# Kernel tuning notes

Hardware: AMD Instinct MI355X
Metric: run time of the kernel (lower is better)

Reference implementation:

```python
import jax, jax.numpy as jnp
import numpy as np

EMBED = 256; DEPTH = 64; DEPTH_START = 1.0
POS_RANGE = (-61.2, -61.2, -10.0, 61.2, 61.2, 10.0)
PC_RANGE = (-51.2, -51.2, -5.0, 51.2, 51.2, 3.0)
MEM_LEN = 512; TOPK = 256; NUM_Q = 900; NUM_CLS = 10; CODE = 10; L = 6
B, N, H, W = 4, 6, 16, 44
PAD_H, PAD_W = 256, 704
TWO_PI = 2.0 * np.pi


def _posemb(coords, nf=128):
    # sine/cosine embedding per coordinate channel -> [..., C, nf]
    dim_t = 10000.0 ** (2.0 * (jnp.arange(nf, dtype=jnp.float32) // 2) / nf)
    p = (coords * TWO_PI)[..., None] / dim_t
    p = jnp.stack([jnp.sin(p[..., 0::2]), jnp.cos(p[..., 1::2])], -1)
    return p.reshape(p.shape[:-2] + (nf,))


def _mlp2(x, W1, b1, W2, b2):
    return jnp.maximum(x @ W1 + b1, 0.0) @ W2 + b2


def _conv1x1(x, Wt, b):
    return jnp.einsum('bchw,co->bohw', x, Wt) + b[None, :, None, None]


def _ln(x, g, b):
    m = jnp.mean(x, -1, keepdims=True)
    v = jnp.mean(jnp.square(x - m), -1, keepdims=True)
    return (x - m) / jnp.sqrt(v + 1e-5) * g + b


def _sine_pe(not_mask):
    # SinePositionalEncoding2D, normalize=True; not_mask: [BN,H,W] float
    nf = EMBED // 2; eps = 1e-6
    y = jnp.cumsum(not_mask, 1); x = jnp.cumsum(not_mask, 2)
    y = y / (y[:, -1:, :] + eps) * TWO_PI
    x = x / (x[:, :, -1:] + eps) * TWO_PI
    dim_t = 10000.0 ** (2.0 * (jnp.arange(nf, dtype=jnp.float32) // 2) / nf)
    px = x[..., None] / dim_t; py = y[..., None] / dim_t
    px = jnp.stack([jnp.sin(px[..., 0::2]), jnp.cos(px[..., 1::2])], -1).reshape(x.shape + (nf,))
    py = jnp.stack([jnp.sin(py[..., 0::2]), jnp.cos(py[..., 1::2])], -1).reshape(y.shape + (nf,))
    return jnp.concatenate([py, px], -1).transpose(0, 3, 1, 2)  # [BN,EMBED,H,W]


def _forward(feat, lidar2img, prev_exists, memory_embedding, memory_reference_point,
             memory_timestamp, outs_dec, ref_pts, ip_w, ip_b, pe_w1, pe_b1, pe_w2, pe_b2,
             ap_w1, ap_b1, ap_w2, ap_b2, qe_w1, qe_b1, qe_w2, qe_b2, te_w1, te_b1, te_w2,
             te_b2, cls_w1, cls_b1, cls_g1, cls_be1, cls_w2, cls_b2, cls_g2, cls_be2,
             cls_w3, cls_b3, reg_w1, reg_b1, reg_w2, reg_b2, reg_w3, reg_b3, masks):
    b, n, c, h, w = feat.shape
    # --- pre_update_memory: memory_refresh + timestamp advance ---
    prev = prev_exists.reshape(b, 1, 1)
    mem_e = memory_embedding * prev
    mem_r = memory_reference_point * prev
    mem_t = memory_timestamp * prev + prev
    # --- input projection (1x1 conv) ---
    x = _conv1x1(feat.reshape(b * n, c, h, w), ip_w, ip_b).reshape(b, n, EMBED, h, w)
    # --- 3D position embedding (PETR frustum) ---
    coords_h = jnp.arange(h, dtype=jnp.float32) * (float(PAD_H) / h)
    coords_w = jnp.arange(w, dtype=jnp.float32) * (float(PAD_W) / w)
    d = jnp.arange(DEPTH, dtype=jnp.float32)
    bin_size = (POS_RANGE[3] - DEPTH_START) / (DEPTH * (1.0 + DEPTH))
    coords_d = DEPTH_START + bin_size * d * (d + 1.0)  # LID discretization
    cw, ch_, cd = jnp.meshgrid(coords_w, coords_h, coords_d, indexing='ij')  # [W,H,D]
    xy = jnp.stack([cw, ch_], -1) * jnp.maximum(cd, 1e-5)[..., None]
    coords4 = jnp.concatenate([xy, cd[..., None], jnp.ones_like(cd[..., None])], -1)  # [W,H,D,4]
    img2lidars = jnp.linalg.inv(lidar2img)  # [B,N,4,4]
    c3 = jnp.einsum('bnij,whdj->bnwhdi', img2lidars, coords4)[..., :3]  # [B,N,W,H,D,3]
    lo = jnp.asarray(POS_RANGE[:3], jnp.float32); hi = jnp.asarray(POS_RANGE[3:], jnp.float32)
    c3 = (c3 - lo) / (hi - lo)
    cmask = ((c3 > 1.0) | (c3 < 0.0)).reshape(b, n, w, h, DEPTH * 3).sum(-1) > DEPTH * 0.5
    coords_mask = masks | cmask.transpose(0, 1, 3, 2)
    c3 = c3.transpose(0, 1, 4, 5, 3, 2).reshape(b * n, DEPTH * 3, h, w)
    c3 = jnp.clip(c3, 0.0, 1.0)
    c3 = jnp.log(jnp.clip(c3, 1e-5, None) / jnp.clip(1.0 - c3, 1e-5, None))  # inverse_sigmoid
    coords_pos = _conv1x1(jnp.maximum(_conv1x1(c3, pe_w1, pe_b1), 0.0), pe_w2, pe_b2)
    coords_pos = coords_pos.reshape(b, n, EMBED, h, w)
    # --- 2D sine PE + adapt_pos3d ---
    sine = _sine_pe((~masks).astype(jnp.float32).reshape(b * n, h, w))
    sine = _conv1x1(jnp.maximum(_conv1x1(sine, ap_w1, ap_b1), 0.0), ap_w2, ap_b2)
    pos_embed = coords_pos + sine.reshape(b, n, EMBED, h, w)
    # --- query / time embeddings ---
    qp = _posemb(ref_pts)  # [Q,3,128]
    qp = jnp.concatenate([qp[:, 1], qp[:, 0], qp[:, 2]], -1)  # (y,x,z) -> [Q,384]
    query_pos = _mlp2(qp, qe_w1, qe_b1, qe_w2, qe_b2)  # [Q,256]
    tp = _posemb(mem_t)[..., 0, :]  # [B,M,128]
    time_emb = _mlp2(tp, te_w1, te_b1, te_w2, te_b2)  # [B,M,256]
    # --- cls / reg branches, stacked over decoder layers ---
    hc = jnp.maximum(_ln(jnp.einsum('lbqd,lde->lbqe', outs_dec, cls_w1) + cls_b1[:, None, None], cls_g1[:, None, None], cls_be1[:, None, None]), 0.0)
    hc = jnp.maximum(_ln(jnp.einsum('lbqd,lde->lbqe', hc, cls_w2) + cls_b2[:, None, None], cls_g2[:, None, None], cls_be2[:, None, None]), 0.0)
    all_cls = jnp.einsum('lbqd,ldc->lbqc', hc, cls_w3) + cls_b3[:, None, None]
    hr = jnp.maximum(jnp.einsum('lbqd,lde->lbqe', outs_dec, reg_w1) + reg_b1[:, None, None], 0.0)
    hr = jnp.maximum(jnp.einsum('lbqd,lde->lbqe', hr, reg_w2) + reg_b2[:, None, None], 0.0)
    all_reg = jnp.einsum('lbqd,ldc->lbqc', hr, reg_w3) + reg_b3[:, None, None]
    # --- post_update_memory: sigmoid + topk + gather + rolling concat ---
    rec_score = jnp.max(jax.nn.sigmoid(all_cls[-1]), -1)  # topk(1) over classes == max
    _, idx = jax.lax.top_k(rec_score, TOPK)  # [B,K]
    rec_mem = jax.lax.stop_gradient(jnp.take_along_axis(outs_dec[-1], idx[..., None], axis=1))
    rec_ref = jax.lax.stop_gradient(jnp.take_along_axis(all_reg[-1][..., :3], idx[..., None], axis=1))
    pmin = jnp.asarray(PC_RANGE[:3], jnp.float32); pmax = jnp.asarray(PC_RANGE[3:], jnp.float32)
    rec_ref = jnp.clip((rec_ref - pmin) / jnp.clip(pmax - pmin, 1e-5, None), 0.0, 1.0)
    rec_ts = jnp.zeros((b, TOPK, 1), rec_mem.dtype)
    new_mem_e = jnp.concatenate([rec_mem, mem_e], 1)[:, :MEM_LEN]
    new_mem_r = jnp.concatenate([rec_ref, mem_r], 1)[:, :MEM_LEN]
    new_mem_t = jnp.concatenate([rec_ts, mem_t], 1)[:, :MEM_LEN]
    return (all_cls, all_reg, new_mem_e, new_mem_r, new_mem_t, pos_embed, x, query_pos, time_emb, coords_mask)


def setup_inputs() -> dict:
    key = jax.random.key(0)
    ks = jax.random.split(key, 24)
    def rn(k, shape, s=0.02):
        return jax.random.normal(k, shape, jnp.float32) * s
    inp = dict(
        feat=jax.random.normal(ks[0], (B, N, 256, H, W), jnp.float32),
        lidar2img=jnp.eye(4, dtype=jnp.float32) + 0.05 * jax.random.normal(ks[1], (B, N, 4, 4), jnp.float32),
        prev_exists=jnp.array([1.0, 0.0, 1.0, 1.0], jnp.float32),
        memory_embedding=jax.random.normal(ks[2], (B, MEM_LEN, EMBED), jnp.float32),
        memory_reference_point=jax.random.uniform(ks[3], (B, MEM_LEN, 3)),
        memory_timestamp=jax.random.uniform(ks[4], (B, MEM_LEN, 1)),
        outs_dec=jax.random.normal(ks[5], (L, B, NUM_Q, EMBED), jnp.float32),
        ref_pts=jax.random.uniform(ks[6], (NUM_Q, 3)),
        ip_w=rn(ks[7], (256, EMBED)), ip_b=jnp.zeros(EMBED),
        pe_w1=rn(ks[8], (3 * DEPTH, EMBED * 2)), pe_b1=jnp.zeros(EMBED * 2),
        pe_w2=rn(ks[9], (EMBED * 2, EMBED)), pe_b2=jnp.zeros(EMBED),
        ap_w1=rn(ks[10], (EMBED, EMBED)), ap_b1=jnp.zeros(EMBED),
        ap_w2=rn(ks[11], (EMBED, EMBED)), ap_b2=jnp.zeros(EMBED),
        qe_w1=rn(ks[12], (EMBED * 3 // 2, EMBED)), qe_b1=jnp.zeros(EMBED),
        qe_w2=rn(ks[13], (EMBED, EMBED)), qe_b2=jnp.zeros(EMBED),
        te_w1=rn(ks[14], (EMBED // 2, EMBED)), te_b1=jnp.zeros(EMBED),
        te_w2=rn(ks[15], (EMBED, EMBED)), te_b2=jnp.zeros(EMBED),
        cls_w1=rn(ks[16], (L, EMBED, EMBED)), cls_b1=jnp.zeros((L, EMBED)),
        cls_g1=jnp.ones((L, EMBED)), cls_be1=jnp.zeros((L, EMBED)),
        cls_w2=rn(ks[17], (L, EMBED, EMBED)), cls_b2=jnp.zeros((L, EMBED)),
        cls_g2=jnp.ones((L, EMBED)), cls_be2=jnp.zeros((L, EMBED)),
        cls_w3=rn(ks[18], (L, EMBED, NUM_CLS)), cls_b3=jnp.zeros((L, NUM_CLS)),
        reg_w1=rn(ks[19], (L, EMBED, EMBED)), reg_b1=jnp.zeros((L, EMBED)),
        reg_w2=rn(ks[20], (L, EMBED, EMBED)), reg_b2=jnp.zeros((L, EMBED)),
        reg_w3=rn(ks[21], (L, EMBED, CODE)), reg_b3=jnp.zeros((L, CODE)),
        masks=jnp.zeros((B, N, H, W), bool),
    )
    return inp


def reference(feat, lidar2img, prev_exists, memory_embedding, memory_reference_point,
              memory_timestamp, outs_dec, ref_pts, ip_w, ip_b, pe_w1, pe_b1, pe_w2, pe_b2,
              ap_w1, ap_b1, ap_w2, ap_b2, qe_w1, qe_b1, qe_w2, qe_b2, te_w1, te_b1, te_w2,
              te_b2, cls_w1, cls_b1, cls_g1, cls_be1, cls_w2, cls_b2, cls_g2, cls_be2,
              cls_w3, cls_b3, reg_w1, reg_b1, reg_w2, reg_b2, reg_w3, reg_b3, masks):
    return _forward(feat, lidar2img, prev_exists, memory_embedding, memory_reference_point,
                    memory_timestamp, outs_dec, ref_pts, ip_w, ip_b, pe_w1, pe_b1, pe_w2, pe_b2,
                    ap_w1, ap_b1, ap_w2, ap_b2, qe_w1, qe_b1, qe_w2, qe_b2, te_w1, te_b1, te_w2,
                    te_b2, cls_w1, cls_b1, cls_g1, cls_be1, cls_w2, cls_b2, cls_g2, cls_be2,
                    cls_w3, cls_b3, reg_w1, reg_b1, reg_w2, reg_b2, reg_w3, reg_b3, masks)
```

## Files before the change

kernel.cpp:

```cpp
#include <hip/hip_runtime.h>
#include <math.h>


typedef unsigned short u16;
typedef __attribute__((ext_vector_type(8))) short short8v;
typedef __attribute__((ext_vector_type(4))) float f32x4;

#define DI __device__ __forceinline__
DI u16 f2bf(float f) {
    unsigned x = __float_as_uint(f);
    return (u16)((x + 0x7fffu + ((x >> 16) & 1u)) >> 16);
}
DI float bf2f(u16 u) { return __uint_as_float(((unsigned)u) << 16); }

#define TWO_PI_F 6.283185307179586f

__global__ void k_inv(const float* __restrict__ l2i, float* __restrict__ out) {
    int t = threadIdx.x;
    if (t >= 24) return;
    float a[4][8];
    for (int i = 0; i < 4; i++)
        for (int j = 0; j < 4; j++) {
            a[i][j] = l2i[t * 16 + i * 4 + j];
            a[i][4 + j] = (i == j) ? 1.f : 0.f;
        }
    for (int c = 0; c < 4; c++) {
        int p = c; float mv = fabsf(a[c][c]);
        for (int r = c + 1; r < 4; r++) {
            float v = fabsf(a[r][c]);
            if (v > mv) { mv = v; p = r; }
        }
        if (p != c)
            for (int j = 0; j < 8; j++) { float tmp = a[c][j]; a[c][j] = a[p][j]; a[p][j] = tmp; }
        float ip = 1.f / a[c][c];
        for (int j = 0; j < 8; j++) a[c][j] *= ip;
        for (int r = 0; r < 4; r++) {
            if (r == c) continue;
            float f = a[r][c];
            for (int j = 0; j < 8; j++) a[r][j] -= f * a[c][j];
        }
    }
    for (int i = 0; i < 4; i++)
        for (int j = 0; j < 4; j++)
            out[t * 16 + i * 4 + j] = a[i][4 + j];
}

__global__ __launch_bounds__(256) void k_memtail(
    const float* __restrict__ me, const float* __restrict__ mr, const float* __restrict__ mt,
    const float* __restrict__ prev,
    float* __restrict__ oe, float* __restrict__ orr, float* __restrict__ ot) {
    int b = blockIdx.x >> 8, j = blockIdx.x & 255, o = threadIdx.x;
    float pv = prev[b];
    oe[(size_t)(b * 512 + 256 + j) * 256 + o] = me[(size_t)(b * 512 + j) * 256 + o] * pv;
    if (o < 3)
        orr[(size_t)(b * 512 + 256 + j) * 3 + o] = mr[(size_t)(b * 512 + j) * 3 + o] * pv;
    if (o == 0) {
        ot[b * 512 + 256 + j] = mt[b * 512 + j] * pv + pv;
        ot[b * 512 + j] = 0.f;
    }
}

__global__ __launch_bounds__(256) void k_frustum(
    const float* __restrict__ inv, u16* __restrict__ c3aT, float* __restrict__ cm) {
    int pix = blockIdx.x * 4 + (threadIdx.x >> 6);
    int d = threadIdx.x & 63;
    int bn = pix / 704, p = pix - bn * 704;
    int h = p / 44, w = p - h * 44;
    const float* M = inv + bn * 16;
    float cw = w * 16.0f, ch = h * 16.0f;
    const float bin = (61.2f - 1.0f) / (64.0f * 65.0f);
    float cd = 1.0f + (bin * d) * (d + 1.0f);
    float xx = cw * cd, yy = ch * cd;
    float px = M[0] * xx + M[1] * yy + M[2] * cd + M[3];
    float py = M[4] * xx + M[5] * yy + M[6] * cd + M[7];
    float pz = M[8] * xx + M[9] * yy + M[10] * cd + M[11];
    float c[3];
    c[0] = (px + 61.2f) * (1.f / 122.4f);
    c[1] = (py + 61.2f) * (1.f / 122.4f);
    c[2] = (pz + 10.0f) * (1.f / 20.0f);
    u16* o = c3aT + (size_t)pix * 192 + d * 3;
    int cnt = 0;
#pragma unroll
    for (int i = 0; i < 3; i++) {
        cnt += ((c[i] > 1.0f) || (c[i] < 0.0f)) ? 1 : 0;
        float cc = fminf(fmaxf(c[i], 0.f), 1.f);
        float num = fmaxf(cc, 1e-5f);
        float den = fmaxf(1.0f - cc, 1e-5f);
        o[i] = f2bf(logf(num / den));
    }
    for (int off = 32; off; off >>= 1) cnt += __shfl_down(cnt, off);
    if (d == 0) cm[pix] = (cnt > 32) ? 1.f : 0.f;
}

__global__ __launch_bounds__(256) void k_sinebase(float* __restrict__ out) {
    int idx = blockIdx.x * 256 + threadIdx.x;
    if (idx >= 256 * 704) return;
    int c = idx / 704, p = idx - c * 704;
    int h = p / 44, w = p - h * 44;
    float pos = (c < 128) ? (h + 1) * (TWO_PI_F / (16.0f + 1e-6f))
                          : (w + 1) * (TWO_PI_F / (44.0f + 1e-6f));
    int cc = c & 127, k = cc >> 1;
    float dt = powf(10000.f, k * (1.f / 64.f));
    float arg = pos / dt;
    out[idx] = (cc & 1) ? cosf(arg) : sinf(arg);
}

template <int MODE>
DI void mlp_body(int blk, const float* __restrict__ src, const float* __restrict__ prev,
                 const float* __restrict__ w1, const float* __restrict__ b1,
                 const float* __restrict__ w2, const float* __restrict__ b2,
                 float* __restrict__ out,
                 float (*finT)[16], float (*h1T)[20], float (*Ws)[256]) {
    constexpr int KF = MODE ? 384 : 128;
    constexpr int T1 = KF / 32;
    constexpr int MROWS = MODE ? 900 : 2048;
    const int tid = threadIdx.x;
    const int r0 = blk * 16;
    const int w4 = (tid >> 6) * 4;
    const int c4 = (tid & 63) * 4;

    for (int i = tid; i < 16 * KF; i += 256) {
        int r = i & 15, f = i >> 4;
        int row = r0 + r;
        int rs = (row < MROWS) ? row : (MROWS - 1);
        float arg;
        int fl;
        if (MODE == 0) {
            float pv = prev[rs >> 9];
            float mt = src[rs] * pv + pv;
            float dt = powf(10000.f, (f >> 1) * (1.f / 64.f));
            arg = mt * TWO_PI_F / dt;
            fl = f;
        } else {
            int seg = f >> 7, ff = f & 127;
            int cidx = (seg == 0) ? 1 : ((seg == 1) ? 0 : 2);
            float rv = src[rs * 3 + cidx];
            float dt = powf(10000.f, (ff >> 1) * (1.f / 64.f));
            arg = rv * TWO_PI_F / dt;
            fl = ff;
        }
        finT[f][r] = (fl & 1) ? cosf(arg) : sinf(arg);
    }

    auto stage = [&](const float* __restrict__ W, int t) {
        const float4* W4 = (const float4*)(W + (size_t)t * 32 * 256);
        float4* S4 = (float4*)Ws;
        float4 tmp[8];
#pragma unroll
        for (int j = 0; j < 8; j++) tmp[j] = W4[tid + j * 256];
#pragma unroll
        for (int j = 0; j < 8; j++) S4[tid + j * 256] = tmp[j];
    };

    float acc1[4][4] = {};
    for (int t = 0; t < T1; t++) {
        stage(w1, t);
        __syncthreads();
#pragma unroll 4
        for (int k = 0; k < 32; k++) {
            float4 fv = *(const float4*)&finT[t * 32 + k][w4];
            float4 wv = *(const float4*)&Ws[k][c4];
            float fa[4] = {fv.x, fv.y, fv.z, fv.w};
            float wa[4] = {wv.x, wv.y, wv.z, wv.w};
#pragma unroll
            for (int i = 0; i < 4; i++)
#pragma unroll
                for (int j = 0; j < 4; j++) acc1[i][j] = fmaf(fa[i], wa[j], acc1[i][j]);
        }
        __syncthreads();
    }
    {
        float4 bv = *(const float4*)&b1[c4];
        float ba[4] = {bv.x, bv.y, bv.z, bv.w};
#pragma unroll
        for (int i = 0; i < 4; i++)
#pragma unroll
            for (int j = 0; j < 4; j++)
                h1T[c4 + j][w4 + i] = fmaxf(acc1[i][j] + ba[j], 0.f);
    }

    float acc2[4][4] = {};
    for (int t = 0; t < 8; t++) {
        stage(w2, t);
        __syncthreads();
#pragma unroll 4
        for (int k = 0; k < 32; k++) {
            float4 fv = *(const float4*)&h1T[t * 32 + k][w4];
            float4 wv = *(const float4*)&Ws[k][c4];
            float fa[4] = {fv.x, fv.y, fv.z, fv.w};
            float wa[4] = {wv.x, wv.y, wv.z, wv.w};
#pragma unroll
            for (int i = 0; i < 4; i++)
#pragma unroll
                for (int j = 0; j < 4; j++) acc2[i][j] = fmaf(fa[i], wa[j], acc2[i][j]);
        }
        __syncthreads();
    }
    {
        float4 bv = *(const float4*)&b2[c4];
#pragma unroll
        for (int i = 0; i < 4; i++) {
            int row = r0 + w4 + i;
            if (row >= MROWS) continue;
            float4 o4;
            o4.x = acc2[i][0] + bv.x;
            o4.y = acc2[i][1] + bv.y;
            o4.z = acc2[i][2] + bv.z;
            o4.w = acc2[i][3] + bv.w;
            *(float4*)&out[(size_t)row * 256 + c4] = o4;
        }
    }
}

__global__ __launch_bounds__(256) void k_mlp2(
    const float* __restrict__ memt, const float* __restrict__ prev,
    const float* __restrict__ te_w1, const float* __restrict__ te_b1,
    const float* __restrict__ te_w2, const float* __restrict__ te_b2,
    float* __restrict__ o_te,
    const float* __restrict__ rp,
    const float* __restrict__ qe_w1, const float* __restrict__ qe_b1,
    const float* __restrict__ qe_w2, const float* __restrict__ qe_b2,
    float* __restrict__ o_qp) {
    __shared__ __align__(16) float finT[384][16];
    __shared__ __align__(16) float h1T[256][20];
    __shared__ __align__(16) float Ws[32][256];
    int blk = blockIdx.x;
    if (blk < 128)
        mlp_body<0>(blk, memt, prev, te_w1, te_b1, te_w2, te_b2, o_te, finT, h1T, Ws);
    else
        mlp_body<1>(blk - 128, rp, prev, qe_w1, qe_b1, qe_w2, qe_b2, o_qp, finT, h1T, Ws);
}

__global__ __launch_bounds__(256) void k_wtr4(
    const float* __restrict__ s0, const float* __restrict__ s1,
    const float* __restrict__ s2, const float* __restrict__ s3,
    u16* __restrict__ d0, u16* __restrict__ d1, u16* __restrict__ d2, u16* __restrict__ d3,
    int K, int N, int zper) {
    __shared__ float sh[32][33];
    int z = blockIdx.z, ti = z / zper, zz = z - ti * zper;
    const float* src = (ti == 0 ? s0 : ti == 1 ? s1 : ti == 2 ? s2 : s3) + (size_t)zz * K * N;
    u16* dst = (ti == 0 ? d0 : ti == 1 ? d1 : ti == 2 ? d2 : d3) + (size_t)zz * K * N;
    int n0 = blockIdx.x * 32, k0 = blockIdx.y * 32;
    int tx = threadIdx.x & 31, ty = threadIdx.x >> 5;
#pragma unroll
    for (int r = 0; r < 4; r++)
        sh[ty + 8 * r][tx] = src[(size_t)(k0 + ty + 8 * r) * N + n0 + tx];
    __syncthreads();
#pragma unroll
    for (int r = 0; r < 4; r++)
        dst[(size_t)(n0 + ty + 8 * r) * K + k0 + tx] = f2bf(sh[tx][ty + 8 * r]);
}

template <int AF32, int BTRANS, int BF32, int OUTF32, int ADD, int BIASM>
__global__ __launch_bounds__(256) void k_mfma(
    const void* __restrict__ Av, const void* __restrict__ B1v, const void* __restrict__ B2v,
    const float* __restrict__ bias1, const float* __restrict__ bias2,
    const float* __restrict__ add, void* __restrict__ outv,
    int M, int N, int K, int lda, int ldb, int ldo,
    long aZ, long bZ, long biasZ, long oZ, int zsplit, int zrelu, int aFull) {
    __shared__ __align__(16) u16 As[64][40];
    __shared__ __align__(16) u16 Bs[128][40];
    const int tid = threadIdx.x;
    const int z = blockIdx.z;
    const int zz = (z < zsplit) ? z : z - zsplit;
    const void* Bv = (z < zsplit) ? B1v : B2v;
    const float* bias = ((z < zsplit) ? bias1 : bias2) + (size_t)zz * biasZ;
    const bool relu = (z >= zrelu);
    const long aOff = (long)(aFull ? z : zz) * aZ;
    const long bOff = (long)zz * bZ;
    const int m0 = blockIdx.y * 64, n0 = blockIdx.x * 128;
    const int wave = tid >> 6, lane = tid & 63, quad = lane >> 4, l16 = lane & 15;
    const int wm = (wave >> 1) * 32, wn = (wave & 1) * 64;
    const int ar = tid & 63, ak = (tid >> 6) << 3;
    const int br = tid & 127, bk = (tid >> 7) << 4;
    f32x4 acc[2][4] = {};

    float pAf[8]; uint4 pAu = make_uint4(0, 0, 0, 0);
    float pBf[16]; u16 pBh[16];
    uint4 pBu0 = make_uint4(0, 0, 0, 0), pBu1 = make_uint4(0, 0, 0, 0);

    auto loadA = [&](int kt) {
        int gm = m0 + ar;
        if (AF32) {
#pragma unroll
            for (int q = 0; q < 8; q++) pAf[q] = 0.f;
            if (gm < M) {
                const float* ap = (const float*)Av + aOff + (size_t)gm * lda + kt + ak;
                float4 f0 = *(const float4*)ap;
                float4 f1 = *(const float4*)(ap + 4);
                pAf[0] = f0.x; pAf[1] = f0.y; pAf[2] = f0.z; pAf[3] = f0.w;
                pAf[4] = f1.x; pAf[5] = f1.y; pAf[6] = f1.z; pAf[7] = f1.w;
            }
        } else {
            pAu = make_uint4(0, 0, 0, 0);
            if (gm < M)
                pAu = *(const uint4*)((const u16*)Av + aOff + (size_t)gm * lda + kt + ak);
        }
    };
    auto storeA = [&]() {
        if (AF32) {
            uint4 u;
            u.x = f2bf(pAf[0]) | ((unsigned)f2bf(pAf[1]) << 16);
            u.y = f2bf(pAf[2]) | ((unsigned)f2bf(pAf[3]) << 16);
            u.z = f2bf(pAf[4]) | ((unsigned)f2bf(pAf[5]) << 16);
            u.w = f2bf(pAf[6]) | ((unsigned)f2bf(pAf[7]) << 16);
            *(uint4*)&As[ar][ak] = u;
        } else {
            *(uint4*)&As[ar][ak] = pAu;
        }
    };
    auto loadB = [&](int kt) {
        int gn = n0 + br;
        if (!BTRANS) {
            pBu0 = make_uint4(0, 0, 0, 0);
            pBu1 = make_uint4(0, 0, 0, 0);
            if (gn < N) {
                const u16* bp = (const u16*)Bv + bOff + (size_t)gn * ldb + kt + bk;
                pBu0 = *(const uint4*)bp;
                pBu1 = *(const uint4*)(bp + 8);
            }
        } else if (BF32) {
#pragma unroll
            for (int kk = 0; kk < 16; kk++)
                pBf[kk] = (gn < N) ? ((const float*)Bv + bOff)[(size_t)(kt + bk + kk) * ldb + gn]
                                   : 0.f;
        } else {
#pragma unroll
            for (int kk = 0; kk < 16; kk++)
                pBh[kk] = (gn < N) ? ((const u16*)Bv + bOff)[(size_t)(kt + bk + kk) * ldb + gn]
                                   : (u16)0;
        }
    };
    auto storeB = [&]() {
        if (!BTRANS) {
            *(uint4*)&Bs[br][bk] = pBu0;
            *(uint4*)&Bs[br][bk + 8] = pBu1;
        } else {
            u16 t[16];
#pragma unroll
            for (int kk = 0; kk < 16; kk++) t[kk] = BF32 ? f2bf(pBf[kk]) : pBh[kk];
            uint4 u0, u1;
            u0.x = t[0] | ((unsigned)t[1] << 16);
            u0.y = t[2] | ((unsigned)t[3] << 16);
            u0.z = t[4] | ((unsigned)t[5] << 16);
            u0.w = t[6] | ((unsigned)t[7] << 16);
            u1.x = t[8] | ((unsigned)t[9] << 16);
            u1.y = t[10] | ((unsigned)t[11] << 16);
            u1.z = t[12] | ((unsigned)t[13] << 16);
            u1.w = t[14] | ((unsigned)t[15] << 16);
            *(uint4*)&Bs[br][bk] = u0;
            *(uint4*)&Bs[br][bk + 8] = u1;
        }
    };

    loadA(0); loadB(0);
    for (int kt = 0; kt < K; kt += 32) {
        storeA(); storeB();
        __syncthreads();
        if (kt + 32 < K) { loadA(kt + 32); loadB(kt + 32); }
        short8v af[2], bfr[4];
#pragma unroll
        for (int i = 0; i < 2; i++) af[i] = *(const short8v*)&As[wm + i * 16 + l16][quad * 8];
#pragma unroll
        for (int j = 0; j < 4; j++) bfr[j] = *(const short8v*)&Bs[wn + j * 16 + l16][quad * 8];
#pragma unroll
        for (int i = 0; i < 2; i++)
#pragma unroll
            for (int j = 0; j < 4; j++)
                acc[i][j] = __builtin_amdgcn_mfma_f32_16x16x32_bf16(af[i], bfr[j], acc[i][j], 0, 0, 0);
        __syncthreads();
    }

    float* outf = (float*)outv + (size_t)z * oZ;
    u16* outh = (u16*)outv + (size_t)z * oZ;
#pragma unroll
    for (int i = 0; i < 2; i++) {
#pragma unroll
        for (int r = 0; r < 4; r++) {
            int row = m0 + wm + i * 16 + quad * 4 + r;
            if (row >= M) continue;
#pragma unroll
            for (int j = 0; j < 4; j++) {
                int col = n0 + wn + j * 16 + l16;
                if (col >= N) continue;
                float v = acc[i][j][r] + (BIASM ? bias[row] : bias[col]);
                if (relu) v = fmaxf(v, 0.f);
                if (ADD) v += add[(size_t)row * ldo + col];
                if (OUTF32) outf[(size_t)row * ldo + col] = v;
                else        outh[(size_t)row * ldo + col] = f2bf(v);
            }
        }
    }
}

__global__ __launch_bounds__(256) void k_sgemm(
    const float* __restrict__ A, const float* __restrict__ Bm,
    const float* __restrict__ bias, float* __restrict__ out, int M) {
    __shared__ __align__(16) float As[16][68];
    __shared__ __align__(16) float Bs[16][68];
    const int tid = threadIdx.x;
    const int m0 = blockIdx.y * 64, n0 = blockIdx.x * 64;
    const int tm = tid >> 4, tn = tid & 15;
    const int kA = tid >> 4, mA = (tid << 2) & 63;
    const int mN = tid & 63, kq = tid >> 6;
    float acc[4][4] = {};
    for (int kt = 0; kt < 256; kt += 16) {
        int gm = m0 + mN;
        float4 u = {0.f, 0.f, 0.f, 0.f};
        if (gm < M) u = *(const float4*)(A + (size_t)gm * 256 + kt + (kq << 2));
        As[(kq << 2) + 0][mN] = u.x; As[(kq << 2) + 1][mN] = u.y;
        As[(kq << 2) + 2][mN] = u.z; As[(kq << 2) + 3][mN] = u.w;
        {
            float4 b = *(const float4*)(Bm + (size_t)(kt + kA) * 256 + n0 + mA);
            Bs[kA][mA + 0] = b.x; Bs[kA][mA + 1] = b.y;
            Bs[kA][mA + 2] = b.z; Bs[kA][mA + 3] = b.w;
        }
        __syncthreads();
#pragma unroll
        for (int k = 0; k < 16; k++) {
            const float4 av = *(const float4*)(&As[k][tm << 2]);
            const float4 bv = *(const float4*)(&Bs[k][tn << 2]);
            float ar[4] = {av.x, av.y, av.z, av.w};
            float br[4] = {bv.x, bv.y, bv.z, bv.w};
#pragma unroll
            for (int i = 0; i < 4; i++)
#pragma unroll
                for (int j = 0; j < 4; j++) acc[i][j] = fmaf(ar[i], br[j], acc[i][j]);
        }
        __syncthreads();
    }
#pragma unroll
    for (int i = 0; i < 4; i++) {
        int row = m0 + (tm << 2) + i;
        if (row >= M) continue;
        float4 o4;
        o4.x = acc[i][0] + bias[n0 + (tn << 2) + 0];
        o4.y = acc[i][1] + bias[n0 + (tn << 2) + 1];
        o4.z = acc[i][2] + bias[n0 + (tn << 2) + 2];
        o4.w = acc[i][3] + bias[n0 + (tn << 2) + 3];
        *(float4*)(out + (size_t)row * 256 + n0 + (tn << 2)) = o4;
    }
}

__global__ __launch_bounds__(256) void k_lnb(
    u16* __restrict__ buf, const float* __restrict__ g, const float* __restrict__ be) {
    int tid = threadIdx.x, wid = tid >> 6, lane = tid & 63;
    int row = blockIdx.x * 4 + wid;
    int l = row / 3600;
    size_t base = (size_t)row * 256 + lane;
    float v[4];
#pragma unroll
    for (int i = 0; i < 4; i++) v[i] = bf2f(buf[base + (i << 6)]);
    float s = v[0] + v[1] + v[2] + v[3];
    for (int off = 32; off; off >>= 1) s += __shfl_down(s, off);
    s = __shfl(s, 0);
    float mean = s * (1.f / 256.f);
    float d[4], q = 0.f;
#pragma unroll
    for (int i = 0; i < 4; i++) { d[i] = v[i] - mean; q += d[i] * d[i]; }
    for (int off = 32; off; off >>= 1) q += __shfl_down(q, off);
    q = __shfl(q, 0);
    float rstd = rsqrtf(q * (1.f / 256.f) + 1e-5f);
#pragma unroll
    for (int i = 0; i < 4; i++) {
        int c = lane + (i << 6);
        buf[base + (i << 6)] = f2bf(fmaxf(d[i] * rstd * g[l * 256 + c] + be[l * 256 + c], 0.f));
    }
}

__global__ __launch_bounds__(256) void k_ln5(
    float* __restrict__ buf, const float* __restrict__ g, const float* __restrict__ be) {
    int tid = threadIdx.x, wid = tid >> 6, lane = tid & 63;
    int row = blockIdx.x * 4 + wid;
    size_t base = (size_t)row * 256 + lane;
    float v[4];
#pragma unroll
    for (int i = 0; i < 4; i++) v[i] = buf[base + (i << 6)];
    float s = v[0] + v[1] + v[2] + v[3];
    for (int off = 32; off; off >>= 1) s += __shfl_down(s, off);
    s = __shfl(s, 0);
    float mean = s * (1.f / 256.f);
    float d[4], q = 0.f;
#pragma unroll
    for (int i = 0; i < 4; i++) { d[i] = v[i] - mean; q += d[i] * d[i]; }
    for (int off = 32; off; off >>= 1) q += __shfl_down(q, off);
    q = __shfl(q, 0);
    float rstd = rsqrtf(q * (1.f / 256.f) + 1e-5f);
#pragma unroll
    for (int i = 0; i < 4; i++) {
        int c = lane + (i << 6);
        buf[base + (i << 6)] = fmaxf(d[i] * rstd * g[c] + be[c], 0.f);
    }
}

__global__ __launch_bounds__(320) void k_heads_cls(
    const u16* __restrict__ hc, const float* __restrict__ wc, const float* __restrict__ bc,
    float* __restrict__ ocls, int lbase) {
    __shared__ u16 sh[32][256];
    int z = blockIdx.z, l = lbase + z, tb = blockIdx.x * 32, tid = threadIdx.x;
    for (int i = tid; i < 8192; i += 320) {
        int rr = i >> 8, k = i & 255;
        int tok = tb + rr;
        sh[rr][k] = (tok < 3600) ? hc[(size_t)(z * 3600 + tok) * 256 + k] : (u16)0;
    }
    __syncthreads();
    int tl = tid / 10, o = tid - tl * 10;
    const float* w = wc + l * 2560 + o;
    float ac = 0.f;
    for (int k = 0; k < 256; k++) ac += bf2f(sh[tl][k]) * w[k * 10];
    ac += bc[l * 10 + o];
    int tok = tb + tl;
    if (tok < 3600) ocls[(size_t)(l * 3600 + tok) * 10 + o] = ac;
}

__global__ __launch_bounds__(320) void k_heads_reg(
    const u16* __restrict__ hr, const float* __restrict__ wr, const float* __restrict__ br,
    float* __restrict__ oreg, float* __restrict__ reg3, int lbase) {
    __shared__ u16 sh[32][256];
    int z = blockIdx.z, l = lbase + z, tb = blockIdx.x * 32, tid = threadIdx.x;
    for (int i = tid; i < 8192; i += 320) {
        int rr = i >> 8, k = i & 255;
        int tok = tb + rr;
        sh[rr][k] = (tok < 3600) ? hr[(size_t)(z * 3600 + tok) * 256 + k] : (u16)0;
    }
    __syncthreads();
    int tl = tid / 10, o = tid - tl * 10;
    const float* w = wr + l * 2560 + o;
    float ar = 0.f;
    for (int k = 0; k < 256; k++) ar += bf2f(sh[tl][k]) * w[k * 10];
    ar += br[l * 10 + o];
    int tok = tb + tl;
    if (tok < 3600) {
        oreg[(size_t)(l * 3600 + tok) * 10 + o] = ar;
        if (l == 5 && o < 3) reg3[tok * 3 + o] = ar;
    }
}

__global__ __launch_bounds__(320) void k_score(
    const float* __restrict__ h2, const float* __restrict__ wc, const float* __restrict__ bc,
    float* __restrict__ score) {
    __shared__ float sh[32][256];
    __shared__ float clsv[32][10];
    int tb = blockIdx.x * 32, tid = threadIdx.x;
    for (int i = tid; i < 8192; i += 320) {
        int rr = i >> 8, k = i & 255;
        int tok = tb + rr;
        sh[rr][k] = (tok < 3600) ? h2[(size_t)tok * 256 + k] : 0.f;
    }
    __syncthreads();
    int tl = tid / 10, o = tid - tl * 10;
    const float* w = wc + 5 * 2560 + o;
    float ac = 0.f;
    for (int k = 0; k < 256; k++) ac += sh[tl][k] * w[k * 10];
    ac += bc[5 * 10 + o];
    int tok = tb + tl;
    if (tok < 3600) clsv[tl][o] = ac;
    __syncthreads();
    if (tid < 32 && tb + tid < 3600) {
        float m = clsv[tid][0];
#pragma unroll
        for (int c = 1; c < 10; c++) m = fmaxf(m, clsv[tid][c]);
        score[tb + tid] = m;
    }
}

__global__ __launch_bounds__(1024) void k_sel(
    const float* __restrict__ score, int* __restrict__ sel) {
    __shared__ float sc[900];
    int b = blockIdx.x, tid = threadIdx.x;
    for (int i = tid; i < 900; i += 1024) sc[i] = score[b * 900 + i];
    __syncthreads();
    if (tid < 900) {
        float s = sc[tid];
        int r = 0;
        for (int j = 0; j < 900; j++) {
            float sj = sc[j];
            r += ((sj > s) || (sj == s && j < tid)) ? 1 : 0;
        }
        if (r < 256) sel[b * 256 + r] = tid;
    }
}

__global__ __launch_bounds__(256) void k_gather(
    const int* __restrict__ sel, const float* __restrict__ reg3,
    const float* __restrict__ od, float* __restrict__ oe, float* __restrict__ orr) {
    int b = blockIdx.y;
    int r = blockIdx.x * 4 + (threadIdx.x >> 6);
    int lane = threadIdx.x & 63;
    int q = sel[b * 256 + r];
    const float4* src = (const float4*)(od + (size_t)((20 + b) * 900 + q) * 256);
    float4* dst = (float4*)(oe + (size_t)(b * 512 + r) * 256);
    dst[lane] = src[lane];
    if (lane == 0) {
#pragma unroll
        for (int kk = 0; kk < 3; kk++) {
            float v = reg3[(b * 900 + q) * 3 + kk];
            float lo = (kk == 2) ? -5.0f : -51.2f;
            float rng = (kk == 2) ? 8.0f : 102.4f;
            orr[(size_t)(b * 512 + r) * 3 + kk] = fminf(fmaxf((v - lo) / rng, 0.f), 1.f);
        }
    }
}

extern "C" void kernel_launch(void* const* d_in, const int* in_sizes, int n_in,
                              void* d_out, int out_size, void* d_ws, size_t ws_size,
                              hipStream_t stream) {
    const float* feat   = (const float*)d_in[0];
    const float* l2i    = (const float*)d_in[1];
    const float* prev   = (const float*)d_in[2];
    const float* meme   = (const float*)d_in[3];
    const float* memr   = (const float*)d_in[4];
    const float* memt   = (const float*)d_in[5];
    const float* od     = (const float*)d_in[6];
    const float* rp     = (const float*)d_in[7];
    const float* ip_w   = (const float*)d_in[8];
    const float* ip_b   = (const float*)d_in[9];
    const float* pe_w1  = (const float*)d_in[10];
    const float* pe_b1  = (const float*)d_in[11];
    const float* pe_w2  = (const float*)d_in[12];
    const float* pe_b2  = (const float*)d_in[13];
    const float* ap_w1  = (const float*)d_in[14];
    const float* ap_b1  = (const float*)d_in[15];
    const float* ap_w2  = (const float*)d_in[16];
    const float* ap_b2  = (const float*)d_in[17];
    const float* qe_w1  = (const float*)d_in[18];
    const float* qe_b1  = (const float*)d_in[19];
    const float* qe_w2  = (const float*)d_in[20];
    const float* qe_b2  = (const float*)d_in[21];
    const float* te_w1  = (const float*)d_in[22];
    const float* te_b1  = (const float*)d_in[23];
    const float* te_w2  = (const float*)d_in[24];
    const float* te_b2  = (const float*)d_in[25];
    const float* cls_w1 = (const float*)d_in[26];
    const float* cls_b1 = (const float*)d_in[27];
    const float* cls_g1 = (const float*)d_in[28];
    const float* cls_be1= (const float*)d_in[29];
    const float* cls_w2 = (const float*)d_in[30];
    const float* cls_b2 = (const float*)d_in[31];
    const float* cls_g2 = (const float*)d_in[32];
    const float* cls_be2= (const float*)d_in[33];
    const float* cls_w3 = (const float*)d_in[34];
    const float* cls_b3 = (const float*)d_in[35];
    const float* reg_w1 = (const float*)d_in[36];
    const float* reg_b1 = (const float*)d_in[37];
    const float* reg_w2 = (const float*)d_in[38];
    const float* reg_b2 = (const float*)d_in[39];
    const float* reg_w3 = (const float*)d_in[40];
    const float* reg_b3 = (const float*)d_in[41];

    float* o32    = (float*)d_out;
    float* o_cls  = o32;
    float* o_reg  = o32 + 216000;
    float* o_meme = o32 + 432000;
    float* o_memr = o32 + 956288;
    float* o_memt = o32 + 962432;
    float* o_pos  = o32 + 964480;
    float* o_x    = o32 + 5289856;
    float* o_qp   = o32 + 9615232;
    float* o_te   = o32 + 9845632;
    float* o_cm   = o32 + 10369920;

    u16*   h1b  = (u16*)(o32 + 432000);
    u16*   h2b  = (u16*)(o32 + 3196800);
    u16*   w1Tc = (u16*)(o32 + 5961600);
    u16*   w1Tr = (u16*)(o32 + 6158208);
    u16*   w2Tc = (u16*)(o32 + 6354816);
    u16*   w2Tr = (u16*)(o32 + 6551424);
    float* h1f  = o32 + 432000;
    float* h2f  = o32 + 1353600;
    u16*   c3aT = (u16*)(o32 + 964480);
    float* sineb = o32 + 432000;
    float* sinea = o32 + 612224;
    u16*   hapb  = (u16*)(o32 + 792448);
    u16*   h1pe  = (u16*)(o32 + 5289856);
    u16*   pe1T  = (u16*)(o32 + 9615232);
    u16*   pe2T  = (u16*)(o32 + 9664384);
    u16*   ap1T  = (u16*)(o32 + 9729920);
    u16*   ap2T  = (u16*)(o32 + 9762688);
    float* w_score = o32 + 9845632;
    float* w_reg3  = o32 + 9849232;
    float* w_inv   = o32 + 9860032;
    int*   w_sel   = (int*)(o32 + 9860416);
    u16*   ipT     = (u16*)(o32 + 9861440);

    k_inv<<<1, 32, 0, stream>>>(l2i, w_inv);

    k_wtr4<<<dim3(8, 8, 24), 256, 0, stream>>>(cls_w1, reg_w1, cls_w2, reg_w2,
                                               w1Tc, w1Tr, w2Tc, w2Tr, 256, 256, 6);
    k_wtr4<<<dim3(16, 6, 1), 256, 0, stream>>>(pe_w1, pe_w1, pe_w1, pe_w1,
                                               pe1T, pe1T, pe1T, pe1T, 192, 512, 1);
    k_wtr4<<<dim3(8, 16, 1), 256, 0, stream>>>(pe_w2, pe_w2, pe_w2, pe_w2,
                                               pe2T, pe2T, pe2T, pe2T, 512, 256, 1);
    k_wtr4<<<dim3(8, 8, 3), 256, 0, stream>>>(ip_w, ap_w1, ap_w2, ap_w2,
                                              ipT, ap1T, ap2T, ap2T, 256, 256, 1);

    k_mfma<1, 0, 0, 0, 0, 0><<<dim3(2, 57, 6), 256, 0, stream>>>(
        od, w1Tc, w1Tc, cls_b1, cls_b1, nullptr, h1b,
        3600, 256, 256, 256, 256, 256, 921600, 65536, 256, 921600, 99, 99, 0);
    k_lnb<<<5400, 256, 0, stream>>>(h1b, cls_g1, cls_be1);
    k_mfma<0, 0, 0, 0, 0, 0><<<dim3(2, 57, 6), 256, 0, stream>>>(
        h1b, w2Tc, w2Tc, cls_b2, cls_b2, nullptr, h2b,
        3600, 256, 256, 256, 256, 256, 921600, 65536, 256, 921600, 99, 99, 1);
    k_lnb<<<5400, 256, 0, stream>>>(h2b, cls_g2, cls_be2);
    k_heads_cls<<<dim3(113, 1, 6), 320, 0, stream>>>(h2b, cls_w3, cls_b3, o_cls, 0);

    k_mfma<1, 0, 0, 0, 0, 0><<<dim3(2, 57, 6), 256, 0, stream>>>(
        od, w1Tr, w1Tr, reg_b1, reg_b1, nullptr, h1b,
        3600, 256, 256, 256, 256, 256, 921600, 65536, 256, 921600, 99, 0, 0);
    k_mfma<0, 0, 0, 0, 0, 0><<<dim3(2, 57, 6), 256, 0, stream>>>(
        h1b, w2Tr, w2Tr, reg_b2, reg_b2, nullptr, h2b,
        3600, 256, 256, 256, 256, 256, 921600, 65536, 256, 921600, 99, 0, 1);
    k_heads_reg<<<dim3(113, 1, 6), 320, 0, stream>>>(h2b, reg_w3, reg_b3, o_reg, w_reg3, 0);

    k_sgemm<<<dim3(4, 57), 256, 0, stream>>>(od + (size_t)5 * 921600, cls_w1 + 5 * 65536,
                                             cls_b1 + 5 * 256, h1f, 3600);
    k_ln5<<<900, 256, 0, stream>>>(h1f, cls_g1 + 5 * 256, cls_be1 + 5 * 256);
    k_sgemm<<<dim3(4, 57), 256, 0, stream>>>(h1f, cls_w2 + 5 * 65536, cls_b2 + 5 * 256, h2f, 3600);
    k_ln5<<<900, 256, 0, stream>>>(h2f, cls_g2 + 5 * 256, cls_be2 + 5 * 256);
    k_score<<<113, 320, 0, stream>>>(h2f, cls_w3, cls_b3, w_score);

    k_frustum<<<4224, 256, 0, stream>>>(w_inv, c3aT, o_cm);
    k_sinebase<<<704, 256, 0, stream>>>(sineb);
    k_mfma<0, 1, 1, 0, 0, 1><<<dim3(6, 4, 1), 256, 0, stream>>>(
        ap1T, sineb, sineb, ap_b1, ap_b1, nullptr, hapb,
        256, 704, 256, 256, 704, 704, 0, 0, 0, 0, 99, 0, 0);
    k_mfma<0, 1, 0, 1, 0, 1><<<dim3(6, 4, 1), 256, 0, stream>>>(
        ap2T, hapb, hapb, ap_b2, ap_b2, nullptr, sinea,
        256, 704, 256, 256, 704, 704, 0, 0, 0, 0, 99, 99, 0);
    k_mfma<0, 0, 0, 0, 0, 1><<<dim3(6, 8, 24), 256, 0, stream>>>(
        pe1T, c3aT, c3aT, pe_b1, pe_b1, nullptr, h1pe,
        512, 704, 192, 192, 192, 704, 0, 135168, 0, 360448, 99, 0, 0);
    k_mfma<0, 1, 0, 1, 1, 1><<<dim3(6, 4, 24), 256, 0, stream>>>(
        pe2T, h1pe, h1pe, pe_b2, pe_b2, sinea, o_pos,
        256, 704, 512, 512, 704, 704, 0, 360448, 0, 180224, 99, 99, 0);
    k_mfma<0, 1, 1, 1, 0, 1><<<dim3(6, 4, 24), 256, 0, stream>>>(
        ipT, feat, feat, ip_b, ip_b, nullptr, o_x,
        256, 704, 256, 256, 704, 704, 0, 180224, 0, 180224, 99, 99, 0);

    k_memtail<<<1024, 256, 0, stream>>>(meme, memr, memt, prev, o_meme, o_memr, o_memt);
    k_sel<<<4, 1024, 0, stream>>>(w_score, w_sel);
    k_gather<<<dim3(64, 4), 256, 0, stream>>>(w_sel, w_reg3, od, o_meme, o_memr);

    k_mlp2<<<185, 256, 0, stream>>>(memt, prev, te_w1, te_b1, te_w2, te_b2, o_te,
                                    rp, qe_w1, qe_b1, qe_w2, qe_b2, o_qp);
}
```

Measured before the change: 593.7 us.

## Pipeline MLP weight loads into registers and compute sine features on the fly

Restructures the fused two-layer MLP kernel so that weights are read straight from global memory into double-buffered registers in 8-row chunks, replacing the shared-memory weight staging. Sine/cosine input features are now produced chunk by chunk, overlapped with compute, instead of being precomputed in one block-wide pass. This cuts shared memory use, which should allow higher occupancy, and hides load latency. In exchange it issues more __syncthreads per block, runs the feature work on only half the threads, and relies on uncoalesced per-thread weight reads being served by cache.

```diff
diff --git a/kernel.cpp b/kernel.cpp
--- a/kernel.cpp
+++ b/kernel.cpp
@@ -110,89 +110,110 @@
                  const float* __restrict__ w1, const float* __restrict__ b1,
                  const float* __restrict__ w2, const float* __restrict__ b2,
                  float* __restrict__ out,
-                 float (*finT)[16], float (*h1T)[20], float (*Ws)[256]) {
+                 float (*finT)[8][16], float (*h1T)[20], float* srcv) {
     constexpr int KF = MODE ? 384 : 128;
-    constexpr int T1 = KF / 32;
+    constexpr int T1 = KF / 8;
+    constexpr int TT = T1 + 32;
     constexpr int MROWS = MODE ? 900 : 2048;
     const int tid = threadIdx.x;
     const int r0 = blk * 16;
     const int w4 = (tid >> 6) * 4;
     const int c4 = (tid & 63) * 4;
 
-    for (int i = tid; i < 16 * KF; i += 256) {
-        int r = i & 15, f = i >> 4;
-        int row = r0 + r;
-        int rs = (row < MROWS) ? row : (MROWS - 1);
-        float arg;
-        int fl;
-        if (MODE == 0) {
+    if (MODE == 0) {
+        if (tid < 16) {
+            int row = r0 + tid;
+            int rs = (row < MROWS) ? row : (MROWS - 1);
             float pv = prev[rs >> 9];
-            float mt = src[rs] * pv + pv;
-            float dt = powf(10000.f, (f >> 1) * (1.f / 64.f));
-            arg = mt * TWO_PI_F / dt;
-            fl = f;
+            srcv[tid] = src[rs] * pv + pv;
+        }
+    } else {
+        if (tid < 48) {
+            int r = tid / 3, c = tid - r * 3;
+            int row = r0 + r;
+            int rs = (row < MROWS) ? row : (MROWS - 1);
+            srcv[r * 3 + c] = src[rs * 3 + c];
+        }
+    }
+
+    float4 wA[8], wB[8];
+    auto wload = [&](float4* w, int t) {
+        const float* W = (t < T1) ? (w1 + (size_t)t * 8 * 256)
+                                  : (w2 + (size_t)(t - T1) * 8 * 256);
+#pragma unroll
+        for (int k = 0; k < 8; k++) w[k] = *(const float4*)&W[k * 256 + c4];
+    };
+    auto features = [&](int t) {
+        if (tid < 128) {
+            int k = tid >> 4, r = tid & 15;
+            int f = t * 8 + k;
+            float arg; int fl;
+            if (MODE == 0) {
+                float dt = powf(10000.f, (f >> 1) * (1.f / 64.f));
+                arg = srcv[r] * TWO_PI_F / dt;
+                fl = f;
+            } else {
+                int seg = f >> 7, ff = f & 127;
+                int cidx = (seg == 0) ? 1 : ((seg == 1) ? 0 : 2);
+                float dt = powf(10000.f, (ff >> 1) * (1.f / 64.f));
+                arg = srcv[r * 3 + cidx] * TWO_PI_F / dt;
+                fl = ff;
+            }
+            finT[t & 1][k][r] = (fl & 1) ? cosf(arg) : sinf(arg);
+        }
+    };
+
+    float acc1[4][4] = {}, acc2[4][4] = {};
+    auto compute = [&](const float4* w, int t) {
+        if (t < T1) {
+#pragma unroll
+            for (int k = 0; k < 8; k++) {
+                float4 fv = *(const float4*)&finT[t & 1][k][w4];
+                float4 wv = w[k];
+                float fa[4] = {fv.x, fv.y, fv.z, fv.w};
+                float wa[4] = {wv.x, wv.y, wv.z, wv.w};
+#pragma unroll
+                for (int i = 0; i < 4; i++)
+#pragma unroll
+                    for (int j = 0; j < 4; j++) acc1[i][j] = fmaf(fa[i], wa[j], acc1[i][j]);
+            }
         } else {
-            int seg = f >> 7, ff = f & 127;
-            int cidx = (seg == 0) ? 1 : ((seg == 1) ? 0 : 2);
-            float rv = src[rs * 3 + cidx];
-            float dt = powf(10000.f, (ff >> 1) * (1.f / 64.f));
-            arg = rv * TWO_PI_F / dt;
-            fl = ff;
-        }
-        finT[f][r] = (fl & 1) ? cosf(arg) : sinf(arg);
-    }
-
-    auto stage = [&](const float* __restrict__ W, int t) {
-        const float4* W4 = (const float4*)(W + (size_t)t * 32 * 256);
-        float4* S4 = (float4*)Ws;
-        float4 tmp[8];
-#pragma unroll
-        for (int j = 0; j < 8; j++) tmp[j] = W4[tid + j * 256];
-#pragma unroll
-        for (int j = 0; j < 8; j++) S4[tid + j * 256] = tmp[j];
+            int tk = (t - T1) * 8;
+#pragma unroll
+            for (int k = 0; k < 8; k++) {
+                float4 fv = *(const float4*)&h1T[tk + k][w4];
+                float4 wv = w[k];
+                float fa[4] = {fv.x, fv.y, fv.z, fv.w};
+                float wa[4] = {wv.x, wv.y, wv.z, wv.w};
+#pragma unroll
+                for (int i = 0; i < 4; i++)
+#pragma unroll
+                    for (int j = 0; j < 4; j++) acc2[i][j] = fmaf(fa[i], wa[j], acc2[i][j]);
+            }
+        }
     };
 
-    float acc1[4][4] = {};
-    for (int t = 0; t < T1; t++) {
-        stage(w1, t);
+    __syncthreads();
+    features(0);
+    wload(wA, 0);
+    __syncthreads();
+
+    for (int t = 0; t < TT; t += 2) {
+        wload(wB, t + 1);
+        if (t + 1 < T1) features(t + 1);
+        compute(wA, t);
         __syncthreads();
-#pragma unroll 4
-        for (int k = 0; k < 32; k++) {
-            float4 fv = *(const float4*)&finT[t * 32 + k][w4];
-            float4 wv = *(const float4*)&Ws[k][c4];
-            float fa[4] = {fv.x, fv.y, fv.z, fv.w};
-            float wa[4] = {wv.x, wv.y, wv.z, wv.w};
+        if (t + 2 < TT) wload(wA, t + 2);
+        if (t + 2 < T1) features(t + 2);
+        compute(wB, t + 1);
+        if (t + 1 == T1 - 1) {
+            float4 bv = *(const float4*)&b1[c4];
+            float ba[4] = {bv.x, bv.y, bv.z, bv.w};
 #pragma unroll
             for (int i = 0; i < 4; i++)
 #pragma unroll
-                for (int j = 0; j < 4; j++) acc1[i][j] = fmaf(fa[i], wa[j], acc1[i][j]);
-        }
-        __syncthreads();
-    }
-    {
-        float4 bv = *(const float4*)&b1[c4];
-        float ba[4] = {bv.x, bv.y, bv.z, bv.w};
-#pragma unroll
-        for (int i = 0; i < 4; i++)
-#pragma unroll
-            for (int j = 0; j < 4; j++)
-                h1T[c4 + j][w4 + i] = fmaxf(acc1[i][j] + ba[j], 0.f);
-    }
-
-    float acc2[4][4] = {};
-    for (int t = 0; t < 8; t++) {
-        stage(w2, t);
-        __syncthreads();
-#pragma unroll 4
-        for (int k = 0; k < 32; k++) {
-            float4 fv = *(const float4*)&h1T[t * 32 + k][w4];
-            float4 wv = *(const float4*)&Ws[k][c4];
-            float fa[4] = {fv.x, fv.y, fv.z, fv.w};
-            float wa[4] = {wv.x, wv.y, wv.z, wv.w};
-#pragma unroll
-            for (int i = 0; i < 4; i++)
-#pragma unroll
-                for (int j = 0; j < 4; j++) acc2[i][j] = fmaf(fa[i], wa[j], acc2[i][j]);
+                for (int j = 0; j < 4; j++)
+                    h1T[c4 + j][w4 + i] = fmaxf(acc1[i][j] + ba[j], 0.f);
         }
         __syncthreads();
     }
@@ -203,10 +224,8 @@
             int row = r0 + w4 + i;
             if (row >= MROWS) continue;
             float4 o4;
-            o4.x = acc2[i][0] + bv.x;
-            o4.y = acc2[i][1] + bv.y;
-            o4.z = acc2[i][2] + bv.z;
-            o4.w = acc2[i][3] + bv.w;
+            o4.x = acc2[i][0] + bv.x; o4.y = acc2[i][1] + bv.y;
+            o4.z = acc2[i][2] + bv.z; o4.w = acc2[i][3] + bv.w;
             *(float4*)&out[(size_t)row * 256 + c4] = o4;
         }
     }
@@ -221,14 +240,14 @@
     const float* __restrict__ qe_w1, const float* __restrict__ qe_b1,
     const float* __restrict__ qe_w2, const float* __restrict__ qe_b2,
     float* __restrict__ o_qp) {
-    __shared__ __align__(16) float finT[384][16];
+    __shared__ __align__(16) float finT[2][8][16];
     __shared__ __align__(16) float h1T[256][20];
-    __shared__ __align__(16) float Ws[32][256];
+    __shared__ __align__(16) float srcv[48];
     int blk = blockIdx.x;
     if (blk < 128)
-        mlp_body<0>(blk, memt, prev, te_w1, te_b1, te_w2, te_b2, o_te, finT, h1T, Ws);
+        mlp_body<0>(blk, memt, prev, te_w1, te_b1, te_w2, te_b2, o_te, finT, h1T, srcv);
     else
-        mlp_body<1>(blk - 128, rp, prev, qe_w1, qe_b1, qe_w2, qe_b2, o_qp, finT, h1T, Ws);
+        mlp_body<1>(blk - 128, rp, prev, qe_w1, qe_b1, qe_w2, qe_b2, o_qp, finT, h1T, srcv);
 }
 
 __global__ __launch_bounds__(256) void k_wtr4(
```

Result: slower. 625.6 us (+5.4%).
